# Kernel tuning notes

Measured on AMD Instinct MI355X. Metric: run time of the kernel, lower is better.

## Reference

```python
import jax, jax.numpy as jnp
import numpy as np


def setup_inputs() -> dict:
    key = jax.random.key(0)
    k1, k2, k3 = jax.random.split(key, 3)
    M, C, N, K, L = 4, 2, 512, 16000, 16
    mixture_w = jax.random.normal(k1, (M, N, K), dtype=jnp.float32)
    est_mask = jax.random.uniform(k2, (M, C, N, K), dtype=jnp.float32)
    W = jax.random.normal(k3, (L, N), dtype=jnp.float32) * (1.0 / np.sqrt(N))
    return {"mixture_w": mixture_w, "est_mask": est_mask, "W": W}


def reference(mixture_w, est_mask, W):
    # mixture_w: [M, N, K]; est_mask: [M, C, N, K]; W: [L, N] (torch Linear weight)
    L = W.shape[0]
    hop = L // 2
    source_w = mixture_w[:, None] * est_mask            # [M, C, N, K]
    frames = jnp.einsum('mcnk,ln->mckl', source_w, W)   # [M, C, K, L]
    M, C, K, Lf = frames.shape
    T = (K - 1) * hop + Lf
    # overlap-and-add: frame k writes to samples [k*hop, k*hop+L)
    idx = (jnp.arange(K)[:, None] * hop + jnp.arange(Lf)[None, :]).reshape(-1)
    est_source = jnp.zeros((M, C, T), frames.dtype).at[:, :, idx].add(
        frames.reshape(M, C, K * Lf))
    return est_source
```

## Files before the change

kernel.cpp:

```cpp
#include <hip/hip_runtime.h>


#define M_   4
#define C_   2
#define N_   512
#define K_   16000
#define L_   16
#define HOP  8
#define T_   ((K_ - 1) * HOP + L_)
#define BK   128
#define NSEG 4
#define NPW  (N_ / NSEG)
#define NB   (K_ / BK)
#define WS_TAIL_OFF (M_ * C_ * NB * 8)

__global__ __launch_bounds__(256, 4)
void decoder_kernel(const float* __restrict__ mix,
                    const float* __restrict__ mask,
                    const float* __restrict__ Wg,
                    float* __restrict__ out,
                    float* __restrict__ ws) {
    __shared__ float lds[6912];

    const int tid  = threadIdx.x;
    const int lane = tid & 63;
    const int w    = tid >> 6;
    const int bidx = blockIdx.x;
    const int c    = bidx & 1;
    const int mk   = bidx >> 1;
    const int m    = mk / NB;
    const int bb   = mk % NB;
    const int k0   = bb * BK;

    float accE[16], accO[16];
    #pragma unroll
    for (int i = 0; i < 16; ++i) { accE[i] = 0.f; accO[i] = 0.f; }

    const int n0w  = w * NPW;
    const int n0wU = __builtin_amdgcn_readfirstlane(n0w);
    const int kk   = k0 + 2 * lane;
    const float* pm = mix  + (size_t)m * N_ * K_ + (size_t)n0w * K_ + kk;
    const float* pk = mask + ((size_t)(m * C_ + c) * N_ + n0w) * K_ + kk;

    #pragma unroll 2
    for (int ch = 0; ch < NPW / 4; ++ch) {
        float2 mv[4], av[4];
        #pragma unroll
        for (int j = 0; j < 4; ++j) {
            mv[j] = *(const float2*)&pm[(size_t)j * K_];
            av[j] = *(const float2*)&pk[(size_t)j * K_];
        }
        float sE[4], sO[4];
        #pragma unroll
        for (int j = 0; j < 4; ++j) {
            sE[j] = mv[j].x * av[j].x;
            sO[j] = mv[j].y * av[j].y;
        }
        const int nbase = n0wU + ch * 4;
        #pragma unroll
        for (int l = 0; l < L_; ++l) {
            const float4 w4 = *(const float4*)&Wg[l * N_ + nbase];
            const float wv[4] = { w4.x, w4.y, w4.z, w4.w };
            #pragma unroll
            for (int j = 0; j < 4; ++j) {
                accE[l] = fmaf(sE[j], wv[j], accE[l]);
                accO[l] = fmaf(sO[j], wv[j], accO[l]);
            }
        }
        pm += (size_t)4 * K_;
        pk += (size_t)4 * K_;
    }

    __syncthreads();
    if (w > 0) {
        float* rb = &lds[(w - 1) * 2304 + lane * 36];
        #pragma unroll
        for (int i = 0; i < 4; ++i)
            *(float4*)&rb[i * 4] = make_float4(accE[i*4], accE[i*4+1],
                                               accE[i*4+2], accE[i*4+3]);
        #pragma unroll
        for (int i = 0; i < 4; ++i)
            *(float4*)&rb[16 + i * 4] = make_float4(accO[i*4], accO[i*4+1],
                                                    accO[i*4+2], accO[i*4+3]);
    }
    __syncthreads();

    if (w == 0) {
        #pragma unroll
        for (int r = 0; r < 3; ++r) {
            const float* rb = &lds[r * 2304 + lane * 36];
            #pragma unroll
            for (int i = 0; i < 4; ++i) {
                const float4 v = *(const float4*)&rb[i * 4];
                accE[i*4]   += v.x;  accE[i*4+1] += v.y;
                accE[i*4+2] += v.z;  accE[i*4+3] += v.w;
            }
            #pragma unroll
            for (int i = 0; i < 4; ++i) {
                const float4 v = *(const float4*)&rb[16 + i * 4];
                accO[i*4]   += v.x;  accO[i*4+1] += v.y;
                accO[i*4+2] += v.z;  accO[i*4+3] += v.w;
            }
        }

        float* ob = out + (size_t)(m * C_ + c) * T_ + (size_t)kk * HOP;
        float cmbE[8], cmbO[8];
        #pragma unroll
        for (int j = 0; j < 8; ++j) {
            const float pv = __shfl_up(accO[8 + j], 1);
            cmbE[j] = accE[j] + pv;
            cmbO[j] = accO[j] + accE[8 + j];
        }
        if (lane == 0) {
            float* hb = ws + (size_t)((m * C_ + c) * NB + bb) * 8;
            *(float4*)&hb[0] = make_float4(accE[0], accE[1], accE[2], accE[3]);
            *(float4*)&hb[4] = make_float4(accE[4], accE[5], accE[6], accE[7]);
        } else {
            *(float4*)&ob[0] = make_float4(cmbE[0], cmbE[1], cmbE[2], cmbE[3]);
            *(float4*)&ob[4] = make_float4(cmbE[4], cmbE[5], cmbE[6], cmbE[7]);
        }
        *(float4*)&ob[8]  = make_float4(cmbO[0], cmbO[1], cmbO[2], cmbO[3]);
        *(float4*)&ob[12] = make_float4(cmbO[4], cmbO[5], cmbO[6], cmbO[7]);
        if (lane == 63) {
            float* tb = ws + WS_TAIL_OFF + (size_t)((m * C_ + c) * NB + bb) * 8;
            *(float4*)&tb[0] = make_float4(accO[8],  accO[9],  accO[10], accO[11]);
            *(float4*)&tb[4] = make_float4(accO[12], accO[13], accO[14], accO[15]);
        }
    }
}

__global__ __launch_bounds__(256)
void boundary_kernel(const float* __restrict__ ws, float* __restrict__ out) {
    const int id = blockIdx.x * 256 + threadIdx.x;
    const int total = M_ * C_ * NB * 8;
    if (id >= total) return;
    const int j  = id & 7;
    const int bb = (id >> 3) % NB;
    const int mc = (id >> 3) / NB;
    float v = ws[(size_t)(mc * NB + bb) * 8 + j];
    if (bb > 0) v += ws[WS_TAIL_OFF + (size_t)(mc * NB + bb - 1) * 8 + j];
    out[(size_t)mc * T_ + (size_t)bb * (BK * HOP) + j] = v;
    if (bb == NB - 1) {
        out[(size_t)mc * T_ + (size_t)K_ * HOP + j] =
            ws[WS_TAIL_OFF + (size_t)(mc * NB + bb) * 8 + j];
    }
}

extern "C" void kernel_launch(void* const* d_in, const int* in_sizes, int n_in,
                              void* d_out, int out_size, void* d_ws, size_t ws_size,
                              hipStream_t stream) {
    const float* mix  = (const float*)d_in[0];
    const float* mask = (const float*)d_in[1];
    const float* Wg   = (const float*)d_in[2];
    float* out = (float*)d_out;
    float* ws  = (float*)d_ws;

    decoder_kernel<<<dim3(M_ * NB * C_), dim3(256), 0, stream>>>(mix, mask, Wg, out, ws);
    boundary_kernel<<<dim3((M_ * C_ * NB * 8 + 255) / 256), dim3(256), 0, stream>>>(ws, out);
}
```

Baseline: 87.11 us.

## Double-buffer loads, use packed float2 FMA, and remap blocks for mix reuse

The main loop now uses explicit register double-buffering, so the next chunk's mix/mask loads are issued before the current chunk is computed. The accumulators become 2-wide vectors so the compiler can emit packed FP32 FMAs (v_pk_fma_f32). The block-index mapping is changed so that groups of 8 consecutive blocks share channel c, which places the c=0 and c=1 blocks of the same (m,bb) 8 blocks apart and should improve L2 reuse of the mixture data. The costs are higher register pressure from the double buffers and a grid padded to a multiple of 16, with an early exit for the extra blocks.

Measured after the change: 84.77 us. -2.7%, faster.

```diff
diff --git a/kernel.cpp b/kernel.cpp
--- a/kernel.cpp
+++ b/kernel.cpp
@@ -11,8 +11,13 @@
 #define BK   128
 #define NSEG 4
 #define NPW  (N_ / NSEG)
+#define NCH  (NPW / 4)
 #define NB   (K_ / BK)
+#define NUNITS (M_ * NB)
+#define GRID ((((NUNITS + 7) / 8) * 16))
 #define WS_TAIL_OFF (M_ * C_ * NB * 8)
+
+typedef float v2f __attribute__((ext_vector_type(2)));
 
 __global__ __launch_bounds__(256, 4)
 void decoder_kernel(const float* __restrict__ mix,
@@ -26,15 +31,16 @@
     const int lane = tid & 63;
     const int w    = tid >> 6;
     const int bidx = blockIdx.x;
-    const int c    = bidx & 1;
-    const int mk   = bidx >> 1;
-    const int m    = mk / NB;
-    const int bb   = mk % NB;
+    const int c    = (bidx >> 3) & 1;
+    const int unit = ((bidx >> 4) << 3) | (bidx & 7);
+    if (unit >= NUNITS) return;
+    const int m    = unit / NB;
+    const int bb   = unit % NB;
     const int k0   = bb * BK;
 
-    float accE[16], accO[16];
+    v2f acc[16];
     #pragma unroll
-    for (int i = 0; i < 16; ++i) { accE[i] = 0.f; accO[i] = 0.f; }
+    for (int i = 0; i < 16; ++i) acc[i] = (v2f)0.f;
 
     const int n0w  = w * NPW;
     const int n0wU = __builtin_amdgcn_readfirstlane(n0w);
@@ -42,46 +48,56 @@
     const float* pm = mix  + (size_t)m * N_ * K_ + (size_t)n0w * K_ + kk;
     const float* pk = mask + ((size_t)(m * C_ + c) * N_ + n0w) * K_ + kk;
 
-    #pragma unroll 2
-    for (int ch = 0; ch < NPW / 4; ++ch) {
-        float2 mv[4], av[4];
-        #pragma unroll
-        for (int j = 0; j < 4; ++j) {
-            mv[j] = *(const float2*)&pm[(size_t)j * K_];
-            av[j] = *(const float2*)&pk[(size_t)j * K_];
-        }
-        float sE[4], sO[4];
-        #pragma unroll
-        for (int j = 0; j < 4; ++j) {
-            sE[j] = mv[j].x * av[j].x;
-            sO[j] = mv[j].y * av[j].y;
-        }
-        const int nbase = n0wU + ch * 4;
-        #pragma unroll
-        for (int l = 0; l < L_; ++l) {
-            const float4 w4 = *(const float4*)&Wg[l * N_ + nbase];
-            const float wv[4] = { w4.x, w4.y, w4.z, w4.w };
-            #pragma unroll
-            for (int j = 0; j < 4; ++j) {
-                accE[l] = fmaf(sE[j], wv[j], accE[l]);
-                accO[l] = fmaf(sO[j], wv[j], accO[l]);
-            }
-        }
-        pm += (size_t)4 * K_;
-        pk += (size_t)4 * K_;
+    v2f mvA[4], avA[4], mvB[4], avB[4];
+
+#define LOAD(MV, AV)                                          \
+    {                                                         \
+        _Pragma("unroll")                                     \
+        for (int j = 0; j < 4; ++j) {                         \
+            MV[j] = *(const v2f*)&pm[(size_t)j * K_];         \
+            AV[j] = *(const v2f*)&pk[(size_t)j * K_];         \
+        }                                                     \
+        pm += (size_t)4 * K_;                                 \
+        pk += (size_t)4 * K_;                                 \
     }
+
+#define COMPUTE(MV, AV, CH)                                   \
+    {                                                         \
+        v2f s[4];                                             \
+        _Pragma("unroll")                                     \
+        for (int j = 0; j < 4; ++j) s[j] = MV[j] * AV[j];     \
+        const int nbase = n0wU + (CH) * 4;                    \
+        _Pragma("unroll")                                     \
+        for (int l = 0; l < L_; ++l) {                        \
+            const float4 w4 = *(const float4*)&Wg[l * N_ + nbase]; \
+            acc[l] += s[0] * w4.x;                            \
+            acc[l] += s[1] * w4.y;                            \
+            acc[l] += s[2] * w4.z;                            \
+            acc[l] += s[3] * w4.w;                            \
+        }                                                     \
+    }
+
+    LOAD(mvA, avA)
+    for (int it = 0; it < NCH - 2; it += 2) {
+        LOAD(mvB, avB)
+        COMPUTE(mvA, avA, it)
+        LOAD(mvA, avA)
+        COMPUTE(mvB, avB, it + 1)
+    }
+    LOAD(mvB, avB)
+    COMPUTE(mvA, avA, NCH - 2)
+    COMPUTE(mvB, avB, NCH - 1)
+
+#undef LOAD
+#undef COMPUTE
 
     __syncthreads();
     if (w > 0) {
         float* rb = &lds[(w - 1) * 2304 + lane * 36];
         #pragma unroll
-        for (int i = 0; i < 4; ++i)
-            *(float4*)&rb[i * 4] = make_float4(accE[i*4], accE[i*4+1],
-                                               accE[i*4+2], accE[i*4+3]);
-        #pragma unroll
-        for (int i = 0; i < 4; ++i)
-            *(float4*)&rb[16 + i * 4] = make_float4(accO[i*4], accO[i*4+1],
-                                                    accO[i*4+2], accO[i*4+3]);
+        for (int i = 0; i < 8; ++i)
+            *(float4*)&rb[i * 4] = make_float4(acc[2*i].x, acc[2*i].y,
+                                               acc[2*i+1].x, acc[2*i+1].y);
     }
     __syncthreads();
 
@@ -90,16 +106,10 @@
         for (int r = 0; r < 3; ++r) {
             const float* rb = &lds[r * 2304 + lane * 36];
             #pragma unroll
-            for (int i = 0; i < 4; ++i) {
+            for (int i = 0; i < 8; ++i) {
                 const float4 v = *(const float4*)&rb[i * 4];
-                accE[i*4]   += v.x;  accE[i*4+1] += v.y;
-                accE[i*4+2] += v.z;  accE[i*4+3] += v.w;
-            }
-            #pragma unroll
-            for (int i = 0; i < 4; ++i) {
-                const float4 v = *(const float4*)&rb[16 + i * 4];
-                accO[i*4]   += v.x;  accO[i*4+1] += v.y;
-                accO[i*4+2] += v.z;  accO[i*4+3] += v.w;
+                acc[2*i].x   += v.x;  acc[2*i].y   += v.y;
+                acc[2*i+1].x += v.z;  acc[2*i+1].y += v.w;
             }
         }
 
@@ -107,14 +117,14 @@
         float cmbE[8], cmbO[8];
         #pragma unroll
         for (int j = 0; j < 8; ++j) {
-            const float pv = __shfl_up(accO[8 + j], 1);
-            cmbE[j] = accE[j] + pv;
-            cmbO[j] = accO[j] + accE[8 + j];
+            const float pv = __shfl_up(acc[8 + j].y, 1);
+            cmbE[j] = acc[j].x + pv;
+            cmbO[j] = acc[j].y + acc[8 + j].x;
         }
         if (lane == 0) {
             float* hb = ws + (size_t)((m * C_ + c) * NB + bb) * 8;
-            *(float4*)&hb[0] = make_float4(accE[0], accE[1], accE[2], accE[3]);
-            *(float4*)&hb[4] = make_float4(accE[4], accE[5], accE[6], accE[7]);
+            *(float4*)&hb[0] = make_float4(acc[0].x, acc[1].x, acc[2].x, acc[3].x);
+            *(float4*)&hb[4] = make_float4(acc[4].x, acc[5].x, acc[6].x, acc[7].x);
         } else {
             *(float4*)&ob[0] = make_float4(cmbE[0], cmbE[1], cmbE[2], cmbE[3]);
             *(float4*)&ob[4] = make_float4(cmbE[4], cmbE[5], cmbE[6], cmbE[7]);
@@ -123,8 +133,8 @@
         *(float4*)&ob[12] = make_float4(cmbO[4], cmbO[5], cmbO[6], cmbO[7]);
         if (lane == 63) {
             float* tb = ws + WS_TAIL_OFF + (size_t)((m * C_ + c) * NB + bb) * 8;
-            *(float4*)&tb[0] = make_float4(accO[8],  accO[9],  accO[10], accO[11]);
-            *(float4*)&tb[4] = make_float4(accO[12], accO[13], accO[14], accO[15]);
+            *(float4*)&tb[0] = make_float4(acc[8].y,  acc[9].y,  acc[10].y, acc[11].y);
+            *(float4*)&tb[4] = make_float4(acc[12].y, acc[13].y, acc[14].y, acc[15].y);
         }
     }
 }
@@ -155,6 +165,6 @@
     float* out = (float*)d_out;
     float* ws  = (float*)d_ws;
 
-    decoder_kernel<<<dim3(M_ * NB * C_), dim3(256), 0, stream>>>(mix, mask, Wg, out, ws);
+    decoder_kernel<<<dim3(GRID), dim3(256), 0, stream>>>(mix, mask, Wg, out, ws);
     boundary_kernel<<<dim3((M_ * C_ * NB * 8 + 255) / 256), dim3(256), 0, stream>>>(ws, out);
 }
```

## Halve the K tile to one frame per lane and swizzle the block-to-channel mapping

Applied to the files above, without the earlier changes.

Each lane now computes a single frame instead of an even/odd pair, so the K tile drops from 128 to 64 frames per block. This halves the accumulator registers and the LDS reduction buffer, and the occupancy hint rises from 4 to 8 blocks per CU. The block index is also remapped so groups of 8 units are processed for one channel before the other, which changes L2 locality for the shared mixture reads. In exchange, global loads narrow from float2 to scalar per lane, and the Wg loads and the cross-wave reduction are spread over twice as many blocks.

Result: faster. 80.78 us (median of 2 runs) (-7.3%).

```diff
diff --git a/kernel.cpp b/kernel.cpp
--- a/kernel.cpp
+++ b/kernel.cpp
@@ -8,64 +8,64 @@
 #define L_   16
 #define HOP  8
 #define T_   ((K_ - 1) * HOP + L_)
-#define BK   128
+#define BK   64
 #define NSEG 4
 #define NPW  (N_ / NSEG)
+#define NCH  (NPW / 4)
 #define NB   (K_ / BK)
+#define NUNITS (M_ * NB)
+#define GRID (NUNITS * C_)
+#define RSTRIDE 20
 #define WS_TAIL_OFF (M_ * C_ * NB * 8)
 
-__global__ __launch_bounds__(256, 4)
+__global__ __launch_bounds__(256, 8)
 void decoder_kernel(const float* __restrict__ mix,
                     const float* __restrict__ mask,
                     const float* __restrict__ Wg,
                     float* __restrict__ out,
                     float* __restrict__ ws) {
-    __shared__ float lds[6912];
+    __shared__ float lds[3 * 64 * RSTRIDE];
 
     const int tid  = threadIdx.x;
     const int lane = tid & 63;
     const int w    = tid >> 6;
     const int bidx = blockIdx.x;
-    const int c    = bidx & 1;
-    const int mk   = bidx >> 1;
-    const int m    = mk / NB;
-    const int bb   = mk % NB;
+    const int c    = (bidx >> 3) & 1;
+    const int unit = ((bidx >> 4) << 3) | (bidx & 7);
+    const int m    = unit / NB;
+    const int bb   = unit % NB;
     const int k0   = bb * BK;
 
-    float accE[16], accO[16];
+    float acc[16];
     #pragma unroll
-    for (int i = 0; i < 16; ++i) { accE[i] = 0.f; accO[i] = 0.f; }
+    for (int i = 0; i < 16; ++i) acc[i] = 0.f;
 
     const int n0w  = w * NPW;
     const int n0wU = __builtin_amdgcn_readfirstlane(n0w);
-    const int kk   = k0 + 2 * lane;
+    const int kk   = k0 + lane;
     const float* pm = mix  + (size_t)m * N_ * K_ + (size_t)n0w * K_ + kk;
     const float* pk = mask + ((size_t)(m * C_ + c) * N_ + n0w) * K_ + kk;
 
     #pragma unroll 2
-    for (int ch = 0; ch < NPW / 4; ++ch) {
-        float2 mv[4], av[4];
+    for (int ch = 0; ch < NCH; ++ch) {
+        float mv[4], av[4];
         #pragma unroll
         for (int j = 0; j < 4; ++j) {
-            mv[j] = *(const float2*)&pm[(size_t)j * K_];
-            av[j] = *(const float2*)&pk[(size_t)j * K_];
+            mv[j] = pm[(size_t)j * K_];
+            av[j] = pk[(size_t)j * K_];
         }
-        float sE[4], sO[4];
+        float s[4];
         #pragma unroll
-        for (int j = 0; j < 4; ++j) {
-            sE[j] = mv[j].x * av[j].x;
-            sO[j] = mv[j].y * av[j].y;
-        }
+        for (int j = 0; j < 4; ++j) s[j] = mv[j] * av[j];
+
         const int nbase = n0wU + ch * 4;
         #pragma unroll
         for (int l = 0; l < L_; ++l) {
             const float4 w4 = *(const float4*)&Wg[l * N_ + nbase];
-            const float wv[4] = { w4.x, w4.y, w4.z, w4.w };
-            #pragma unroll
-            for (int j = 0; j < 4; ++j) {
-                accE[l] = fmaf(sE[j], wv[j], accE[l]);
-                accO[l] = fmaf(sO[j], wv[j], accO[l]);
-            }
+            acc[l] = fmaf(s[0], w4.x, acc[l]);
+            acc[l] = fmaf(s[1], w4.y, acc[l]);
+            acc[l] = fmaf(s[2], w4.z, acc[l]);
+            acc[l] = fmaf(s[3], w4.w, acc[l]);
         }
         pm += (size_t)4 * K_;
         pk += (size_t)4 * K_;
@@ -73,58 +73,45 @@
 
     __syncthreads();
     if (w > 0) {
-        float* rb = &lds[(w - 1) * 2304 + lane * 36];
+        float* rb = &lds[(w - 1) * (64 * RSTRIDE) + lane * RSTRIDE];
         #pragma unroll
         for (int i = 0; i < 4; ++i)
-            *(float4*)&rb[i * 4] = make_float4(accE[i*4], accE[i*4+1],
-                                               accE[i*4+2], accE[i*4+3]);
-        #pragma unroll
-        for (int i = 0; i < 4; ++i)
-            *(float4*)&rb[16 + i * 4] = make_float4(accO[i*4], accO[i*4+1],
-                                                    accO[i*4+2], accO[i*4+3]);
+            *(float4*)&rb[i * 4] = make_float4(acc[i*4], acc[i*4+1],
+                                               acc[i*4+2], acc[i*4+3]);
     }
     __syncthreads();
 
     if (w == 0) {
         #pragma unroll
         for (int r = 0; r < 3; ++r) {
-            const float* rb = &lds[r * 2304 + lane * 36];
+            const float* rb = &lds[r * (64 * RSTRIDE) + lane * RSTRIDE];
             #pragma unroll
             for (int i = 0; i < 4; ++i) {
                 const float4 v = *(const float4*)&rb[i * 4];
-                accE[i*4]   += v.x;  accE[i*4+1] += v.y;
-                accE[i*4+2] += v.z;  accE[i*4+3] += v.w;
-            }
-            #pragma unroll
-            for (int i = 0; i < 4; ++i) {
-                const float4 v = *(const float4*)&rb[16 + i * 4];
-                accO[i*4]   += v.x;  accO[i*4+1] += v.y;
-                accO[i*4+2] += v.z;  accO[i*4+3] += v.w;
+                acc[i*4]   += v.x;  acc[i*4+1] += v.y;
+                acc[i*4+2] += v.z;  acc[i*4+3] += v.w;
             }
         }
 
         float* ob = out + (size_t)(m * C_ + c) * T_ + (size_t)kk * HOP;
-        float cmbE[8], cmbO[8];
+        float cmb[8];
         #pragma unroll
         for (int j = 0; j < 8; ++j) {
-            const float pv = __shfl_up(accO[8 + j], 1);
-            cmbE[j] = accE[j] + pv;
-            cmbO[j] = accO[j] + accE[8 + j];
+            const float pv = __shfl_up(acc[8 + j], 1);
+            cmb[j] = acc[j] + pv;
         }
         if (lane == 0) {
             float* hb = ws + (size_t)((m * C_ + c) * NB + bb) * 8;
-            *(float4*)&hb[0] = make_float4(accE[0], accE[1], accE[2], accE[3]);
-            *(float4*)&hb[4] = make_float4(accE[4], accE[5], accE[6], accE[7]);
+            *(float4*)&hb[0] = make_float4(acc[0], acc[1], acc[2], acc[3]);
+            *(float4*)&hb[4] = make_float4(acc[4], acc[5], acc[6], acc[7]);
         } else {
-            *(float4*)&ob[0] = make_float4(cmbE[0], cmbE[1], cmbE[2], cmbE[3]);
-            *(float4*)&ob[4] = make_float4(cmbE[4], cmbE[5], cmbE[6], cmbE[7]);
+            *(float4*)&ob[0] = make_float4(cmb[0], cmb[1], cmb[2], cmb[3]);
+            *(float4*)&ob[4] = make_float4(cmb[4], cmb[5], cmb[6], cmb[7]);
         }
-        *(float4*)&ob[8]  = make_float4(cmbO[0], cmbO[1], cmbO[2], cmbO[3]);
-        *(float4*)&ob[12] = make_float4(cmbO[4], cmbO[5], cmbO[6], cmbO[7]);
         if (lane == 63) {
             float* tb = ws + WS_TAIL_OFF + (size_t)((m * C_ + c) * NB + bb) * 8;
-            *(float4*)&tb[0] = make_float4(accO[8],  accO[9],  accO[10], accO[11]);
-            *(float4*)&tb[4] = make_float4(accO[12], accO[13], accO[14], accO[15]);
+            *(float4*)&tb[0] = make_float4(acc[8],  acc[9],  acc[10], acc[11]);
+            *(float4*)&tb[4] = make_float4(acc[12], acc[13], acc[14], acc[15]);
         }
     }
 }
@@ -155,6 +142,6 @@
     float* out = (float*)d_out;
     float* ws  = (float*)d_ws;
 
-    decoder_kernel<<<dim3(M_ * NB * C_), dim3(256), 0, stream>>>(mix, mask, Wg, out, ws);
+    decoder_kernel<<<dim3(GRID), dim3(256), 0, stream>>>(mix, mask, Wg, out, ws);
     boundary_kernel<<<dim3((M_ * C_ * NB * 8 + 255) / 256), dim3(256), 0, stream>>>(ws, out);
 }
```
